# Kernel optimization log

Measured on AMD Instinct MI355X. Metric: run time of the kernel, lower is better.

Reference implementation:

```python
import jax, jax.numpy as jnp
import numpy as np


def get_rel_pos(q_size, k_size, rel_pos):
    # sizes are static python ints; rel_pos has length 2*max(q_size,k_size)-1
    q_ratio = max(k_size / q_size, 1.0)
    k_ratio = max(q_size / k_size, 1.0)
    dist = (np.arange(q_size)[:, None] * q_ratio
            - (np.arange(k_size)[None, :] + (1.0 - k_size)) * k_ratio).astype(np.int64)
    return rel_pos[dist]  # [q_size, k_size, head_dim]


def decomposed_rel_pos_3d(qh, q_thw, k_thw, rel_pos_t, rel_pos_h, rel_pos_w):
    # qh: [B, Q, n_heads, head_dim]
    q_t, q_h, q_w = q_thw
    k_t, k_h, k_w = k_thw
    Rt = get_rel_pos(q_t, k_t, rel_pos_t)
    Rh = get_rel_pos(q_h, k_h, rel_pos_h)
    Rw = get_rel_pos(q_w, k_w, rel_pos_w)
    B = qh.shape[0]
    n, c = qh.shape[2], qh.shape[3]
    q6 = qh.reshape(B, q_t, q_h, q_w, n, c)
    rel_t = jnp.einsum('bthwnc,tkc->bnthwk', q6, Rt)
    rel_h = jnp.einsum('bthwnc,hkc->bnthwk', q6, Rh)
    rel_w = jnp.einsum('bthwnc,wkc->bnthwk', q6, Rw)
    bias = (rel_t[:, :, :, :, :, :, None, None]
            + rel_h[:, :, :, :, :, None, :, None]
            + rel_w[:, :, :, :, :, None, None, :])
    return bias.reshape(B, n, q_t * q_h * q_w, k_t * k_h * k_w)


def setup_inputs() -> dict:
    key = jax.random.key(0)
    ks = jax.random.split(key, 16)
    B, dim, num_heads = 2, 768, 12
    head_dim = dim // num_heads
    q_thw = (8, 14, 14)
    k_thw = (8, 14, 14)
    Q = q_thw[0] * q_thw[1] * q_thw[2]
    K = k_thw[0] * k_thw[1] * k_thw[2]
    s = 0.02
    inp = {
        'q': jax.random.normal(ks[0], (B, Q, dim), jnp.float32),
        'k': jax.random.normal(ks[1], (B, K, dim), jnp.float32),
        'Wq': jax.random.normal(ks[2], (dim, dim), jnp.float32) * s,
        'bq': jnp.zeros((dim,), jnp.float32),
        'Wk': jax.random.normal(ks[3], (dim, dim), jnp.float32) * s,
        'bk': jnp.zeros((dim,), jnp.float32),
        'Wv': jax.random.normal(ks[4], (dim, dim), jnp.float32) * s,
        'bv': jnp.zeros((dim,), jnp.float32),
        'Wo': jax.random.normal(ks[5], (dim, dim), jnp.float32) * s,
        'bo': jnp.zeros((dim,), jnp.float32),
        'rel_pos_t': jax.random.normal(ks[6], (2 * max(q_thw[0], k_thw[0]) - 1, head_dim), jnp.float32) * s,
        'rel_pos_h': jax.random.normal(ks[7], (2 * max(q_thw[1], k_thw[1]) - 1, head_dim), jnp.float32) * s,
        'rel_pos_w': jax.random.normal(ks[8], (2 * max(q_thw[2], k_thw[2]) - 1, head_dim), jnp.float32) * s,
        'q_t': q_thw[0], 'q_h': q_thw[1], 'q_w': q_thw[2],
        'k_t': k_thw[0], 'k_h': k_thw[1], 'k_w': k_thw[2],
    }
    return inp


def reference(q, k, Wq, bq, Wk, bk, Wv, bv, Wo, bo,
              rel_pos_t, rel_pos_h, rel_pos_w,
              q_t, q_h, q_w, k_t, k_h, k_w):
    B, Q, dim = q.shape
    num_heads = 12
    c = dim // num_heads
    scale = 1.0 / np.sqrt(c).astype(np.float32)
    qh = (q @ Wq.T + bq).reshape(B, -1, num_heads, c)   # [B,Q,n,c]
    vh = (k @ Wv.T + bv).reshape(B, -1, num_heads, c)   # [B,K,n,c]
    kh = (k @ Wk.T + bk).reshape(B, -1, num_heads, c)   # [B,K,n,c]
    bias = decomposed_rel_pos_3d(qh, (q_t, q_h, q_w), (k_t, k_h, k_w),
                                 rel_pos_t, rel_pos_h, rel_pos_w)  # [B,n,Q,K]
    scores = jnp.einsum('bqnc,bknc->bnqk', qh, kh) * scale + bias
    attn = jax.nn.softmax(scores, axis=-1)
    out = jnp.einsum('bnqk,bknc->bqnc', attn, vh).reshape(B, Q, dim)
    return out @ Wo.T + bo
```

## Files before the change

### kernel.cpp

```cpp
#include <hip/hip_runtime.h>
#include <math.h>

typedef __bf16 bf16_t;
typedef __bf16 bf16x4 __attribute__((ext_vector_type(4)));
typedef __bf16 bf16x8 __attribute__((ext_vector_type(8)));
typedef float floatx4 __attribute__((ext_vector_type(4)));

#define MFMA16(A, B, C) __builtin_amdgcn_mfma_f32_16x16x32_bf16((A), (B), (C), 0, 0, 0)

static constexpr int BB  = 2;
static constexpr int NH  = 12;
static constexpr int HD  = 64;
static constexpr int DIM = 768;
static constexpr int QS  = 1568;
static constexpr int KS  = 1568;
static constexpr int KSP = 1664;
static constexpr int MROWS = BB * QS;
static constexpr int KT  = 32;
static constexpr int TD  = 80;

static constexpr float LOG2E = 1.4426950408889634f;
static constexpr float SCALE_L2E = 0.125f * LOG2E;

__device__ __forceinline__ void async16(const void* g, void* l) {
    __builtin_amdgcn_global_load_lds(
        (const __attribute__((address_space(1))) unsigned int*)g,
        (__attribute__((address_space(3))) unsigned int*)l, 16, 0, 0);
}

__global__ __launch_bounds__(256) void cvt_w(
    const float* __restrict__ q, const float* __restrict__ k,
    const float* __restrict__ wq, const float* __restrict__ wk,
    const float* __restrict__ wv, const float* __restrict__ wo,
    const float* __restrict__ rpt, const float* __restrict__ rph,
    const float* __restrict__ rpw,
    bf16_t* __restrict__ Wb, bf16_t* __restrict__ qb, bf16_t* __restrict__ kb,
    bf16_t* __restrict__ koh, bf16_t* __restrict__ Tt)
{
    const int NW4 = DIM * DIM / 4;
    const int NX4 = MROWS * DIM / 4;
    int i = blockIdx.x * 256 + threadIdx.x;
    if (i < 4 * NW4) {
        const int w = i / NW4;
        const int off = i - w * NW4;
        const float* src = (w == 0) ? wq : (w == 1) ? wk : (w == 2) ? wv : wo;
        floatx4 v = ((const floatx4*)src)[off];
        bf16x4 o;
#pragma unroll
        for (int r = 0; r < 4; ++r) o[r] = (bf16_t)v[r];
        ((bf16x4*)(Wb + (size_t)w * DIM * DIM))[off] = o;
        return;
    }
    i -= 4 * NW4;
    if (i < 2 * NX4) {
        const float* src = (i < NX4) ? q : k;
        bf16_t* dst = (i < NX4) ? qb : kb;
        const int off = (i < NX4) ? i : i - NX4;
        floatx4 v = ((const floatx4*)src)[off];
        bf16x4 o;
#pragma unroll
        for (int r = 0; r < 4; ++r) o[r] = (bf16_t)v[r];
        ((bf16x4*)dst)[off] = o;
        return;
    }
    i -= 2 * NX4;
    if (i < KS) {
        const int key = i;
        const int tk = key / 196;
        const int rem = key - tk * 196;
        const int hk = rem / 14;
        const int wk_ = rem - hk * 14;
#pragma unroll
        for (int c8 = 0; c8 < 8; ++c8) {
            bf16x8 v;
#pragma unroll
            for (int j = 0; j < 8; ++j) {
                const int e = c8 * 8 + j;
                const float f = (e == tk || e == 8 + hk || e == 22 + wk_) ? 1.f : 0.f;
                v[j] = (bf16_t)f;
            }
            *(bf16x8*)(koh + (size_t)key * 64 + c8 * 8) = v;
        }
        return;
    }
    i -= KS;
    if (i < TD * 8) {
        const int d = i >> 3;
        const int c8 = (i & 7) * 8;
        bf16x8 v;
#pragma unroll
        for (int j = 0; j < 8; ++j) {
            const int c = c8 + j;
            float f = 0.f;
            if (d < 15)      f = LOG2E * rpt[(size_t)d * 64 + c];
            else if (d < 42) f = LOG2E * rph[(size_t)(d - 15) * 64 + c];
            else if (d < 69) f = LOG2E * rpw[(size_t)(d - 42) * 64 + c];
            v[j] = (bf16_t)f;
        }
        *(bf16x8*)(Tt + (size_t)d * 64 + c8) = v;
    }
}

__global__ __launch_bounds__(256) void gemm_qkv(
    const bf16_t* __restrict__ qb, const bf16_t* __restrict__ kb,
    const bf16_t* __restrict__ Wb,
    const float* __restrict__ bq, const float* __restrict__ bk,
    const float* __restrict__ bv,
    bf16_t* __restrict__ qhP, bf16_t* __restrict__ khP, bf16_t* __restrict__ vT)
{
    __shared__ __align__(16) bf16_t Asa[128 * 64];
    __shared__ __align__(16) bf16_t Asb[128 * 64];
    __shared__ __align__(16) bf16_t Bsa[64 * 64];
    __shared__ __align__(16) bf16_t Bsb[64 * 64];

    const int tid   = threadIdx.x;
    const int lane  = tid & 63;
    const int wave  = tid >> 6;
    const int row16 = lane & 15;
    const int quad  = lane >> 4;
    const int wm    = wave & 1;
    const int wn    = wave >> 1;
    const int m0 = blockIdx.x * 128;
    const int yb = blockIdx.y;
    const int proj = yb / 12;
    const int n0 = (yb - proj * 12) * 64;

    const bf16_t* X = (proj == 0) ? qb : kb;
    const bf16_t* W = Wb + (size_t)proj * DIM * DIM;
    const float* bias = (proj == 0) ? bq : (proj == 1) ? bk : bv;
    const float osc = (proj == 1) ? SCALE_L2E : 1.0f;

    floatx4 acc[4][2];
#pragma unroll
    for (int mt = 0; mt < 4; ++mt)
#pragma unroll
        for (int nt = 0; nt < 2; ++nt) acc[mt][nt] = (floatx4){0.f, 0.f, 0.f, 0.f};

    auto stage = [&](int k0, bf16_t* An, bf16_t* Bn) {
#pragma unroll
        for (int p = 0; p < 4; ++p) {
            const int s = p * 256 + tid;
            const int row = s >> 3, c = s & 7;
            const int g = c ^ (row & 7);
            const int rowc = min(m0 + row, MROWS - 1);
            async16(X + (size_t)rowc * DIM + k0 + g * 8, An + s * 8);
        }
#pragma unroll
        for (int p = 0; p < 2; ++p) {
            const int s = p * 256 + tid;
            const int row = s >> 3, c = s & 7;
            const int g = c ^ (row & 7);
            async16(W + (size_t)(n0 + row) * DIM + k0 + g * 8, Bn + s * 8);
        }
    };

    auto body = [&](int k0, const bf16_t* Ac, const bf16_t* Bc,
                    bf16_t* An, bf16_t* Bn, bool pf) {
        __syncthreads();
        if (pf) stage(k0 + 64, An, Bn);
#pragma unroll
        for (int h = 0; h < 2; ++h) {
            const int pa = (h * 4 + quad) ^ (row16 & 7);
            bf16x8 aF[4], bF[2];
#pragma unroll
            for (int mt = 0; mt < 4; ++mt) {
                const int rowA = wm * 64 + mt * 16 + row16;
                aF[mt] = *(const bf16x8*)&Ac[rowA * 64 + pa * 8];
            }
#pragma unroll
            for (int nt = 0; nt < 2; ++nt) {
                const int rowB = wn * 32 + nt * 16 + row16;
                bF[nt] = *(const bf16x8*)&Bc[rowB * 64 + pa * 8];
            }
#pragma unroll
            for (int mt = 0; mt < 4; ++mt)
#pragma unroll
                for (int nt = 0; nt < 2; ++nt)
                    acc[mt][nt] = MFMA16(aF[mt], bF[nt], acc[mt][nt]);
        }
    };

    stage(0, Asa, Bsa);
    for (int ii = 0; ii < 6; ++ii) {
        const int k0 = ii * 128;
        body(k0,      Asa, Bsa, Asb, Bsb, true);
        body(k0 + 64, Asb, Bsb, Asa, Bsa, k0 + 128 < DIM);
    }

#pragma unroll
    for (int nt = 0; nt < 2; ++nt) {
        const int col = n0 + wn * 32 + nt * 16 + row16;
        const int head = col >> 6, cl = col & 63;
        const float bv_ = bias[col];
#pragma unroll
        for (int mt = 0; mt < 4; ++mt) {
            const int row0 = m0 + wm * 64 + mt * 16 + quad * 4;
            if (row0 < MROWS) {
                const int bb = (row0 >= KS) ? 1 : 0;
                const int key0 = row0 - bb * KS;
                if (proj == 2) {
                    bf16x4 pv;
#pragma unroll
                    for (int r = 0; r < 4; ++r) pv[r] = (bf16_t)(acc[mt][nt][r] + bv_);
                    *(bf16x4*)&vT[((size_t)(bb * NH + head) * 64 + cl) * KSP + key0] = pv;
                } else {
                    bf16_t* dst = (proj == 0) ? qhP : khP;
#pragma unroll
                    for (int r = 0; r < 4; ++r)
                        dst[((size_t)(bb * NH + head) * KS + key0 + r) * 64 + cl] =
                            (bf16_t)((acc[mt][nt][r] + bv_) * osc);
                }
            }
        }
    }
}

__global__ __launch_bounds__(256) void qext(
    const bf16_t* __restrict__ qhP, const bf16_t* __restrict__ Tt,
    bf16_t* __restrict__ Qe)
{
    __shared__ float Gs[64][81];

    const int tid   = threadIdx.x;
    const int lane  = tid & 63;
    const int wave  = tid >> 6;
    const int row16 = lane & 15;
    const int quad  = lane >> 4;
    const int m0 = blockIdx.x * 64;

    const bf16_t* ap = qhP + (size_t)(m0 + wave * 16 + row16) * 64 + quad * 8;
    bf16x8 a0 = *(const bf16x8*)(ap);
    bf16x8 a1 = *(const bf16x8*)(ap + 32);

    floatx4 acc[5];
#pragma unroll
    for (int t = 0; t < 5; ++t) {
        const bf16_t* tp = Tt + (size_t)(t * 16 + row16) * 64 + quad * 8;
        floatx4 s = (floatx4){0.f, 0.f, 0.f, 0.f};
        s = MFMA16(a0, *(const bf16x8*)(tp), s);
        s = MFMA16(a1, *(const bf16x8*)(tp + 32), s);
        acc[t] = s;
    }
#pragma unroll
    for (int t = 0; t < 5; ++t)
#pragma unroll
        for (int r = 0; r < 4; ++r)
            Gs[wave * 16 + quad * 4 + r][t * 16 + row16] = acc[t][r];
    __syncthreads();

#pragma unroll
    for (int ii = 0; ii < 16; ++ii) {
        const int i = ii * 256 + tid;
        const int row = i >> 6, e = i & 63;
        const int grow = m0 + row;
        const int qg = grow % QS;
        const int tq = qg / 196;
        const int rem = qg - tq * 196;
        const int hq = rem / 14;
        const int wq = rem - hq * 14;
        int d;
        if (e < 8)       d = tq - e + 7;
        else if (e < 22) d = 15 + hq - (e - 8) + 13;
        else             d = 42 + wq - (e - 22) + 13;
        const float val = (e < 36) ? Gs[row][d] : 0.f;
        Qe[(size_t)grow * 64 + e] = (bf16_t)val;
    }
}

__global__ __launch_bounds__(256, 2) void attn_fused(
    const bf16_t* __restrict__ qhP, const bf16_t* __restrict__ Qe,
    const bf16_t* __restrict__ khP, const bf16_t* __restrict__ koh,
    const bf16_t* __restrict__ vT, bf16_t* __restrict__ ao)
{
    __shared__ __align__(16) bf16_t KsA[32 * 128];
    __shared__ __align__(16) bf16_t KsB[32 * 128];
    __shared__ __align__(16) bf16_t VsA[64 * 32];
    __shared__ __align__(16) bf16_t VsB[64 * 32];
    __shared__ __align__(16) bf16_t Pl[4 * 16 * 40];

    const int tid   = threadIdx.x;
    const int lane  = tid & 63;
    const int wave  = tid >> 6;
    const int row16 = lane & 15;
    const int quad  = lane >> 4;

    const int L = blockIdx.x;
    const int xcd = L & 7;
    const int j = L >> 3;
    const int bn = xcd * 3 + (j % 3);
    const int q0 = (j / 3) * 64;
    const int b = bn / NH;
    const int n = bn - b * NH;

    const int qrow = min(q0 + wave * 16 + row16, QS - 1);
    const bf16_t* qp = qhP + ((size_t)bn * QS + qrow) * 64 + quad * 8;
    const bf16_t* qe = Qe  + ((size_t)bn * QS + qrow) * 64 + quad * 8;
    bf16x8 aQ0 = *(const bf16x8*)(qp);
    bf16x8 aQ1 = *(const bf16x8*)(qp + 32);
    bf16x8 aQ2 = *(const bf16x8*)(qe);
    bf16x8 aQ3 = *(const bf16x8*)(qe + 32);

    floatx4 O[4];
#pragma unroll
    for (int ct = 0; ct < 4; ++ct) O[ct] = (floatx4){0.f, 0.f, 0.f, 0.f};
    float lsum[4] = {0.f, 0.f, 0.f, 0.f};

    const bf16_t* khb = khP + (size_t)bn * KS * 64;
    const bf16_t* vTb = vT + (size_t)bn * 64 * KSP;
    const int pbase = wave * 16 * 40;
    const int sw3 = row16 & 7;
    const int sw2 = (row16 >> 1) & 3;

    auto stageKV = [&](int k0, bf16_t* Kn, bf16_t* Vn) {
#pragma unroll
        for (int p = 0; p < 2; ++p) {
            const int s = p * 256 + tid;
            const int row = s >> 4, c = s & 15;
            const int l = c ^ (row & 7);
            const bf16_t* src = (l < 8)
                ? khb + (size_t)(k0 + row) * 64 + l * 8
                : koh + (size_t)(k0 + row) * 64 + (l - 8) * 8;
            async16(src, Kn + s * 8);
        }
        {
            const int row = tid >> 2, c = tid & 3;
            const int l = c ^ ((row >> 1) & 3);
            async16(vTb + (size_t)row * KSP + k0 + l * 8, Vn + tid * 8);
        }
    };

    auto iter = [&](int ki, const bf16_t* Kc, const bf16_t* Vc,
                    bf16_t* Kn, bf16_t* Vn, bool pf) {
        const int k0 = ki * KT;
        __syncthreads();
        if (pf) stageKV(k0 + KT, Kn, Vn);

        floatx4 S[2];
#pragma unroll
        for (int t = 0; t < 2; ++t) {
            const bf16_t* kp_ = &Kc[(t * 16 + row16) * 128];
            floatx4 s = (floatx4){0.f, 0.f, 0.f, 0.f};
            s = MFMA16(aQ0, *(const bf16x8*)&kp_[((0 + quad) ^ sw3) * 8], s);
            s = MFMA16(aQ1, *(const bf16x8*)&kp_[((4 + quad) ^ sw3) * 8], s);
            s = MFMA16(aQ2, *(const bf16x8*)&kp_[((8 + quad) ^ sw3) * 8], s);
            s = MFMA16(aQ3, *(const bf16x8*)&kp_[((12 + quad) ^ sw3) * 8], s);
            S[t] = s;
        }

#pragma unroll
        for (int t = 0; t < 2; ++t) {
#pragma unroll
            for (int r = 0; r < 4; ++r) {
                float p = __builtin_amdgcn_exp2f(S[t][r]);
                lsum[r] += p;
                Pl[pbase + (quad * 4 + r) * 40 + t * 16 + row16] = (bf16_t)p;
            }
        }

        bf16x8 aP = *(const bf16x8*)&Pl[pbase + row16 * 40 + quad * 8];
#pragma unroll
        for (int ct = 0; ct < 4; ++ct) {
            bf16x8 bV = *(const bf16x8*)&Vc[(ct * 16 + row16) * 32 + (quad ^ sw2) * 8];
            O[ct] = MFMA16(aP, bV, O[ct]);
        }
    };

    stageKV(0, KsA, VsA);
#pragma unroll 1
    for (int kp2 = 0; kp2 < 24; ++kp2) {
        iter(2 * kp2,     KsA, VsA, KsB, VsB, true);
        iter(2 * kp2 + 1, KsB, VsB, KsA, VsA, true);
    }
    iter(48, KsA, VsA, KsB, VsB, false);

    float inv[4];
#pragma unroll
    for (int r = 0; r < 4; ++r) {
        float l = lsum[r];
        l += __shfl_xor(l, 1);
        l += __shfl_xor(l, 2);
        l += __shfl_xor(l, 4);
        l += __shfl_xor(l, 8);
        inv[r] = 1.f / l;
    }
#pragma unroll
    for (int ct = 0; ct < 4; ++ct) {
        const int c = n * HD + ct * 16 + row16;
#pragma unroll
        for (int r = 0; r < 4; ++r) {
            const int qr = q0 + wave * 16 + quad * 4 + r;
            if (qr < QS)
                ao[(size_t)(b * QS + qr) * DIM + c] = (bf16_t)(O[ct][r] * inv[r]);
        }
    }
}

__global__ __launch_bounds__(256) void gemm_o(
    const bf16_t* __restrict__ X, const bf16_t* __restrict__ W,
    const float* __restrict__ bias, float* __restrict__ Y)
{
    __shared__ __align__(16) bf16_t Asa[64 * 64];
    __shared__ __align__(16) bf16_t Asb[64 * 64];
    __shared__ __align__(16) bf16_t Bsa[64 * 64];
    __shared__ __align__(16) bf16_t Bsb[64 * 64];

    const int tid   = threadIdx.x;
    const int lane  = tid & 63;
    const int wave  = tid >> 6;
    const int row16 = lane & 15;
    const int quad  = lane >> 4;
    const int m0 = blockIdx.x * 64;
    const int n0 = blockIdx.y * 64;

    floatx4 acc[4];
#pragma unroll
    for (int nt = 0; nt < 4; ++nt) acc[nt] = (floatx4){0.f, 0.f, 0.f, 0.f};

    auto stage = [&](int k0, bf16_t* An, bf16_t* Bn) {
#pragma unroll
        for (int p = 0; p < 2; ++p) {
            const int s = p * 256 + tid;
            const int row = s >> 3, pc = s & 7;
            const int g = pc ^ (row & 7);
            async16(X + (size_t)(m0 + row) * DIM + k0 + g * 8, An + s * 8);
            async16(W + (size_t)(n0 + row) * DIM + k0 + g * 8, Bn + s * 8);
        }
    };

    auto body = [&](int k0, const bf16_t* Ac, const bf16_t* Bc,
                    bf16_t* An, bf16_t* Bn, bool pf) {
        __syncthreads();
        if (pf) stage(k0 + 64, An, Bn);
#pragma unroll
        for (int h = 0; h < 2; ++h) {
            const int lc = h * 4 + quad;
            const int pa = lc ^ (row16 & 7);
            const int rowA = wave * 16 + row16;
            bf16x8 aF = *(const bf16x8*)&Ac[rowA * 64 + pa * 8];
#pragma unroll
            for (int nt = 0; nt < 4; ++nt) {
                bf16x8 bF = *(const bf16x8*)&Bc[(nt * 16 + row16) * 64 + pa * 8];
                acc[nt] = MFMA16(aF, bF, acc[nt]);
            }
        }
    };

    stage(0, Asa, Bsa);
    for (int ii = 0; ii < 6; ++ii) {
        const int k0 = ii * 128;
        body(k0,      Asa, Bsa, Asb, Bsb, true);
        body(k0 + 64, Asb, Bsb, Asa, Bsa, k0 + 128 < DIM);
    }

#pragma unroll
    for (int nt = 0; nt < 4; ++nt) {
        const int col = n0 + nt * 16 + row16;
        const float bv = bias[col];
#pragma unroll
        for (int r = 0; r < 4; ++r) {
            const int row = m0 + wave * 16 + quad * 4 + r;
            Y[(size_t)row * DIM + col] = acc[nt][r] + bv;
        }
    }
}

extern "C" void kernel_launch(void* const* d_in, const int* in_sizes, int n_in,
                              void* d_out, int out_size, void* d_ws, size_t ws_size,
                              hipStream_t stream) {
    const float* q   = (const float*)d_in[0];
    const float* k   = (const float*)d_in[1];
    const float* Wq  = (const float*)d_in[2];
    const float* bq  = (const float*)d_in[3];
    const float* Wk  = (const float*)d_in[4];
    const float* bk  = (const float*)d_in[5];
    const float* Wv  = (const float*)d_in[6];
    const float* bv  = (const float*)d_in[7];
    const float* Wo  = (const float*)d_in[8];
    const float* bo  = (const float*)d_in[9];
    const float* rpt = (const float*)d_in[10];
    const float* rph = (const float*)d_in[11];
    const float* rpw = (const float*)d_in[12];

    bf16_t* qhP  = (bf16_t*)d_ws;
    bf16_t* khP  = qhP  + (size_t)MROWS * DIM;
    bf16_t* vT   = khP  + (size_t)MROWS * DIM;
    bf16_t* QeKb = vT   + (size_t)BB * NH * HD * KSP;
    bf16_t* aoQb = QeKb + (size_t)MROWS * DIM;
    bf16_t* koh  = aoQb + (size_t)MROWS * DIM;
    bf16_t* Tt   = koh  + (size_t)KS * 64;
    bf16_t* Wb   = Tt   + (size_t)TD * 64;

    const int NW4 = DIM * DIM / 4;
    const int NX4 = MROWS * DIM / 4;
    const int NCVT = 4 * NW4 + 2 * NX4 + KS + TD * 8;
    cvt_w<<<(NCVT + 255) / 256, 256, 0, stream>>>(
        q, k, Wq, Wk, Wv, Wo, rpt, rph, rpw, Wb, aoQb, QeKb, koh, Tt);

    gemm_qkv<<<dim3(25, 36), 256, 0, stream>>>(
        aoQb, QeKb, Wb, bq, bk, bv, qhP, khP, vT);

    qext<<<(BB * NH * QS) / 64, 256, 0, stream>>>(qhP, Tt, QeKb);

    attn_fused<<<dim3(8 * 3 * 25), 256, 0, stream>>>(
        qhP, QeKb, khP, koh, vT, aoQb);

    gemm_o<<<dim3(MROWS / 64, DIM / 64), 256, 0, stream>>>(
        aoQb, Wb + (size_t)3 * DIM * DIM, bo, (float*)d_out);
}
```

Baseline: 206.3 us.

## Widen attention key tile to 64 with 2x2 wave split and LDS reduction

The fused attention kernel now processes 64 keys per step instead of 32. Each wave handles 32 query rows by 32 keys, so every K fragment loaded from LDS feeds two query row groups and every V fragment feeds two MFMAs. Partial O and row sums from the two key-group waves are merged through LDS at the end. Keys past the sequence end are clamped on load and masked to zero probability, and the padded tail of V^T is zeroed in the conversion kernel. The aim is fewer barriers and more operand reuse, at the cost of more LDS per block, higher register pressure, and an extra reduction step.

```diff
diff --git a/kernel.cpp b/kernel.cpp
--- a/kernel.cpp
+++ b/kernel.cpp
@@ -16,7 +16,7 @@
 static constexpr int KS  = 1568;
 static constexpr int KSP = 1664;
 static constexpr int MROWS = BB * QS;
-static constexpr int KT  = 32;
+static constexpr int KT  = 64;
 static constexpr int TD  = 80;
 
 static constexpr float LOG2E = 1.4426950408889634f;
@@ -35,10 +35,11 @@
     const float* __restrict__ rpt, const float* __restrict__ rph,
     const float* __restrict__ rpw,
     bf16_t* __restrict__ Wb, bf16_t* __restrict__ qb, bf16_t* __restrict__ kb,
-    bf16_t* __restrict__ koh, bf16_t* __restrict__ Tt)
+    bf16_t* __restrict__ koh, bf16_t* __restrict__ Tt, bf16_t* __restrict__ vT)
 {
     const int NW4 = DIM * DIM / 4;
     const int NX4 = MROWS * DIM / 4;
+    const int PADC = (KSP - KS) / 8;
     int i = blockIdx.x * 256 + threadIdx.x;
     if (i < 4 * NW4) {
         const int w = i / NW4;
@@ -98,6 +99,16 @@
             v[j] = (bf16_t)f;
         }
         *(bf16x8*)(Tt + (size_t)d * 64 + c8) = v;
+        return;
+    }
+    i -= TD * 8;
+    if (i < BB * NH * HD * PADC) {
+        const int row = i / PADC;
+        const int ch  = i - row * PADC;
+        bf16x8 z;
+#pragma unroll
+        for (int r = 0; r < 8; ++r) z[r] = (bf16_t)0.f;
+        *(bf16x8*)(vT + (size_t)row * KSP + KS + ch * 8) = z;
     }
 }
 
@@ -272,17 +283,19 @@
     const bf16_t* __restrict__ khP, const bf16_t* __restrict__ koh,
     const bf16_t* __restrict__ vT, bf16_t* __restrict__ ao)
 {
-    __shared__ __align__(16) bf16_t KsA[32 * 128];
-    __shared__ __align__(16) bf16_t KsB[32 * 128];
-    __shared__ __align__(16) bf16_t VsA[64 * 32];
-    __shared__ __align__(16) bf16_t VsB[64 * 32];
-    __shared__ __align__(16) bf16_t Pl[4 * 16 * 40];
+    __shared__ __align__(16) bf16_t KsA[64 * 128];
+    __shared__ __align__(16) bf16_t KsB[64 * 128];
+    __shared__ __align__(16) bf16_t VsA[64 * 64];
+    __shared__ __align__(16) bf16_t VsB[64 * 64];
+    __shared__ __align__(16) bf16_t Pl[4 * 16 * 72];
 
     const int tid   = threadIdx.x;
     const int lane  = tid & 63;
     const int wave  = tid >> 6;
     const int row16 = lane & 15;
     const int quad  = lane >> 4;
+    const int qg    = wave & 1;
+    const int kg    = wave >> 1;
 
     const int L = blockIdx.x;
     const int xcd = L & 7;
@@ -292,40 +305,48 @@
     const int b = bn / NH;
     const int n = bn - b * NH;
 
-    const int qrow = min(q0 + wave * 16 + row16, QS - 1);
-    const bf16_t* qp = qhP + ((size_t)bn * QS + qrow) * 64 + quad * 8;
-    const bf16_t* qe = Qe  + ((size_t)bn * QS + qrow) * 64 + quad * 8;
-    bf16x8 aQ0 = *(const bf16x8*)(qp);
-    bf16x8 aQ1 = *(const bf16x8*)(qp + 32);
-    bf16x8 aQ2 = *(const bf16x8*)(qe);
-    bf16x8 aQ3 = *(const bf16x8*)(qe + 32);
-
-    floatx4 O[4];
-#pragma unroll
-    for (int ct = 0; ct < 4; ++ct) O[ct] = (floatx4){0.f, 0.f, 0.f, 0.f};
-    float lsum[4] = {0.f, 0.f, 0.f, 0.f};
+    bf16x8 aQ[2][4];
+#pragma unroll
+    for (int rg = 0; rg < 2; ++rg) {
+        const int qrow = min(q0 + qg * 32 + rg * 16 + row16, QS - 1);
+        const bf16_t* qp = qhP + ((size_t)bn * QS + qrow) * 64 + quad * 8;
+        const bf16_t* qe = Qe  + ((size_t)bn * QS + qrow) * 64 + quad * 8;
+        aQ[rg][0] = *(const bf16x8*)(qp);
+        aQ[rg][1] = *(const bf16x8*)(qp + 32);
+        aQ[rg][2] = *(const bf16x8*)(qe);
+        aQ[rg][3] = *(const bf16x8*)(qe + 32);
+    }
+
+    floatx4 O[2][4];
+#pragma unroll
+    for (int rg = 0; rg < 2; ++rg)
+#pragma unroll
+        for (int ct = 0; ct < 4; ++ct) O[rg][ct] = (floatx4){0.f, 0.f, 0.f, 0.f};
+    float lsum[2][4] = {{0.f, 0.f, 0.f, 0.f}, {0.f, 0.f, 0.f, 0.f}};
 
     const bf16_t* khb = khP + (size_t)bn * KS * 64;
     const bf16_t* vTb = vT + (size_t)bn * 64 * KSP;
-    const int pbase = wave * 16 * 40;
-    const int sw3 = row16 & 7;
-    const int sw2 = (row16 >> 1) & 3;
+    const int rsw = row16 & 7;
+    const int pbase = qg * 2 * 16 * 72;
 
     auto stageKV = [&](int k0, bf16_t* Kn, bf16_t* Vn) {
 #pragma unroll
-        for (int p = 0; p < 2; ++p) {
+        for (int p = 0; p < 4; ++p) {
             const int s = p * 256 + tid;
             const int row = s >> 4, c = s & 15;
             const int l = c ^ (row & 7);
+            const int rowc = min(k0 + row, KS - 1);
             const bf16_t* src = (l < 8)
-                ? khb + (size_t)(k0 + row) * 64 + l * 8
-                : koh + (size_t)(k0 + row) * 64 + (l - 8) * 8;
+                ? khb + (size_t)rowc * 64 + l * 8
+                : koh + (size_t)rowc * 64 + (l - 8) * 8;
             async16(src, Kn + s * 8);
         }
-        {
-            const int row = tid >> 2, c = tid & 3;
-            const int l = c ^ ((row >> 1) & 3);
-            async16(vTb + (size_t)row * KSP + k0 + l * 8, Vn + tid * 8);
+#pragma unroll
+        for (int p = 0; p < 2; ++p) {
+            const int s = p * 256 + tid;
+            const int row = s >> 3, c = s & 7;
+            const int l = c ^ (row & 7);
+            async16(vTb + (size_t)row * KSP + k0 + l * 8, Vn + s * 8);
         }
     };
 
@@ -335,63 +356,109 @@
         __syncthreads();
         if (pf) stageKV(k0 + KT, Kn, Vn);
 
-        floatx4 S[2];
+        floatx4 S[2][2];
 #pragma unroll
         for (int t = 0; t < 2; ++t) {
-            const bf16_t* kp_ = &Kc[(t * 16 + row16) * 128];
-            floatx4 s = (floatx4){0.f, 0.f, 0.f, 0.f};
-            s = MFMA16(aQ0, *(const bf16x8*)&kp_[((0 + quad) ^ sw3) * 8], s);
-            s = MFMA16(aQ1, *(const bf16x8*)&kp_[((4 + quad) ^ sw3) * 8], s);
-            s = MFMA16(aQ2, *(const bf16x8*)&kp_[((8 + quad) ^ sw3) * 8], s);
-            s = MFMA16(aQ3, *(const bf16x8*)&kp_[((12 + quad) ^ sw3) * 8], s);
-            S[t] = s;
+            const int krow = kg * 32 + t * 16 + row16;
+            const bf16_t* kp_ = &Kc[krow * 128];
+            bf16x8 kf[4];
+#pragma unroll
+            for (int c = 0; c < 4; ++c)
+                kf[c] = *(const bf16x8*)&kp_[((c * 4 + quad) ^ rsw) * 8];
+#pragma unroll
+            for (int rg = 0; rg < 2; ++rg) {
+                floatx4 s = (floatx4){0.f, 0.f, 0.f, 0.f};
+                s = MFMA16(aQ[rg][0], kf[0], s);
+                s = MFMA16(aQ[rg][1], kf[1], s);
+                s = MFMA16(aQ[rg][2], kf[2], s);
+                s = MFMA16(aQ[rg][3], kf[3], s);
+                S[rg][t] = s;
+            }
         }
 
 #pragma unroll
         for (int t = 0; t < 2; ++t) {
-#pragma unroll
-            for (int r = 0; r < 4; ++r) {
-                float p = __builtin_amdgcn_exp2f(S[t][r]);
-                lsum[r] += p;
-                Pl[pbase + (quad * 4 + r) * 40 + t * 16 + row16] = (bf16_t)p;
-            }
-        }
-
-        bf16x8 aP = *(const bf16x8*)&Pl[pbase + row16 * 40 + quad * 8];
+            const int key = k0 + kg * 32 + t * 16 + row16;
+            const bool ok = (key < KS);
+#pragma unroll
+            for (int rg = 0; rg < 2; ++rg) {
+#pragma unroll
+                for (int r = 0; r < 4; ++r) {
+                    float p = __builtin_amdgcn_exp2f(S[rg][t][r]);
+                    p = ok ? p : 0.f;
+                    lsum[rg][r] += p;
+                    Pl[pbase + rg * 1152 + (quad * 4 + r) * 72 + kg * 32 + t * 16 + row16]
+                        = (bf16_t)p;
+                }
+            }
+        }
+
+        bf16x8 aP[2];
+#pragma unroll
+        for (int rg = 0; rg < 2; ++rg)
+            aP[rg] = *(const bf16x8*)&Pl[pbase + rg * 1152 + row16 * 72 + kg * 32 + quad * 8];
 #pragma unroll
         for (int ct = 0; ct < 4; ++ct) {
-            bf16x8 bV = *(const bf16x8*)&Vc[(ct * 16 + row16) * 32 + (quad ^ sw2) * 8];
-            O[ct] = MFMA16(aP, bV, O[ct]);
+            const bf16x8 bV =
+                *(const bf16x8*)&Vc[(ct * 16 + row16) * 64 + ((kg * 4 + quad) ^ rsw) * 8];
+            O[0][ct] = MFMA16(aP[0], bV, O[0][ct]);
+            O[1][ct] = MFMA16(aP[1], bV, O[1][ct]);
         }
     };
 
     stageKV(0, KsA, VsA);
 #pragma unroll 1
-    for (int kp2 = 0; kp2 < 24; ++kp2) {
+    for (int kp2 = 0; kp2 < 12; ++kp2) {
         iter(2 * kp2,     KsA, VsA, KsB, VsB, true);
         iter(2 * kp2 + 1, KsB, VsB, KsA, VsA, true);
     }
-    iter(48, KsA, VsA, KsB, VsB, false);
-
-    float inv[4];
-#pragma unroll
-    for (int r = 0; r < 4; ++r) {
-        float l = lsum[r];
-        l += __shfl_xor(l, 1);
-        l += __shfl_xor(l, 2);
-        l += __shfl_xor(l, 4);
-        l += __shfl_xor(l, 8);
-        inv[r] = 1.f / l;
-    }
-#pragma unroll
-    for (int ct = 0; ct < 4; ++ct) {
-        const int c = n * HD + ct * 16 + row16;
-#pragma unroll
-        for (int r = 0; r < 4; ++r) {
-            const int qr = q0 + wave * 16 + quad * 4 + r;
-            if (qr < QS)
-                ao[(size_t)(b * QS + qr) * DIM + c] = (bf16_t)(O[ct][r] * inv[r]);
-        }
+    iter(24, KsA, VsA, KsB, VsB, false);
+
+    __syncthreads();
+    float* Oex = (float*)KsA;
+    float* Lex = (float*)VsA;
+    if (kg == 1) {
+#pragma unroll
+        for (int rg = 0; rg < 2; ++rg) {
+#pragma unroll
+            for (int ct = 0; ct < 4; ++ct)
+                *(floatx4*)&Oex[((qg * 64 + lane) * 8 + rg * 4 + ct) * 4] = O[rg][ct];
+#pragma unroll
+            for (int r = 0; r < 4; ++r)
+                Lex[(qg * 64 + lane) * 8 + rg * 4 + r] = lsum[rg][r];
+        }
+    }
+    __syncthreads();
+    if (kg == 0) {
+        float inv[2][4];
+#pragma unroll
+        for (int rg = 0; rg < 2; ++rg) {
+#pragma unroll
+            for (int ct = 0; ct < 4; ++ct)
+                O[rg][ct] += *(const floatx4*)&Oex[((qg * 64 + lane) * 8 + rg * 4 + ct) * 4];
+#pragma unroll
+            for (int r = 0; r < 4; ++r) {
+                float l = lsum[rg][r] + Lex[(qg * 64 + lane) * 8 + rg * 4 + r];
+                l += __shfl_xor(l, 1);
+                l += __shfl_xor(l, 2);
+                l += __shfl_xor(l, 4);
+                l += __shfl_xor(l, 8);
+                inv[rg][r] = 1.f / l;
+            }
+        }
+#pragma unroll
+        for (int rg = 0; rg < 2; ++rg)
+#pragma unroll
+            for (int ct = 0; ct < 4; ++ct) {
+                const int c = n * HD + ct * 16 + row16;
+#pragma unroll
+                for (int r = 0; r < 4; ++r) {
+                    const int qr = q0 + qg * 32 + rg * 16 + quad * 4 + r;
+                    if (qr < QS)
+                        ao[(size_t)(b * QS + qr) * DIM + c] =
+                            (bf16_t)(O[rg][ct][r] * inv[rg][r]);
+                }
+            }
     }
 }
 
@@ -492,9 +559,10 @@
 
     const int NW4 = DIM * DIM / 4;
     const int NX4 = MROWS * DIM / 4;
-    const int NCVT = 4 * NW4 + 2 * NX4 + KS + TD * 8;
+    const int PADC = (KSP - KS) / 8;
+    const int NCVT = 4 * NW4 + 2 * NX4 + KS + TD * 8 + BB * NH * HD * PADC;
     cvt_w<<<(NCVT + 255) / 256, 256, 0, stream>>>(
-        q, k, Wq, Wk, Wv, Wo, rpt, rph, rpw, Wb, aoQb, QeKb, koh, Tt);
+        q, k, Wq, Wk, Wv, Wo, rpt, rph, rpw, Wb, aoQb, QeKb, koh, Tt, vT);
 
     gemm_qkv<<<dim3(25, 36), 256, 0, stream>>>(
         aoQb, QeKb, Wb, bq, bk, bv, qhP, khP, vT);
```

Result: slower. 211.5 us (+2.5%).

## Halve attention block to 32 query rows with 128 threads and split MFMA chains

Applied to the files above, without the earlier changes.

The attention kernel now uses 2 waves covering 32 query rows per block instead of 4 waves covering 64, so it launches 49 row tiles per head instead of 25 and drops the partial last tile and its bounds checks, since 1568 divides evenly by 32. The QK^T accumulation is split into two independent MFMA chains to shorten the dependency latency. The V padding columns are now zeroed explicitly in the conversion kernel. The smaller blocks are meant to improve occupancy and load balance across CUs, at the cost of reloading each K/V tile from memory twice as often.

```diff
diff --git a/kernel.cpp b/kernel.cpp
--- a/kernel.cpp
+++ b/kernel.cpp
@@ -35,10 +35,11 @@
     const float* __restrict__ rpt, const float* __restrict__ rph,
     const float* __restrict__ rpw,
     bf16_t* __restrict__ Wb, bf16_t* __restrict__ qb, bf16_t* __restrict__ kb,
-    bf16_t* __restrict__ koh, bf16_t* __restrict__ Tt)
+    bf16_t* __restrict__ koh, bf16_t* __restrict__ Tt, bf16_t* __restrict__ vT)
 {
     const int NW4 = DIM * DIM / 4;
     const int NX4 = MROWS * DIM / 4;
+    const int PADC = (KSP - KS) / 8;
     int i = blockIdx.x * 256 + threadIdx.x;
     if (i < 4 * NW4) {
         const int w = i / NW4;
@@ -98,6 +99,16 @@
             v[j] = (bf16_t)f;
         }
         *(bf16x8*)(Tt + (size_t)d * 64 + c8) = v;
+        return;
+    }
+    i -= TD * 8;
+    if (i < BB * NH * HD * PADC) {
+        const int row = i / PADC;
+        const int ch  = i - row * PADC;
+        bf16x8 z;
+#pragma unroll
+        for (int r = 0; r < 8; ++r) z[r] = (bf16_t)0.f;
+        *(bf16x8*)(vT + (size_t)row * KSP + KS + ch * 8) = z;
     }
 }
 
@@ -267,7 +278,7 @@
     }
 }
 
-__global__ __launch_bounds__(256, 2) void attn_fused(
+__global__ __launch_bounds__(128, 3) void attn_fused(
     const bf16_t* __restrict__ qhP, const bf16_t* __restrict__ Qe,
     const bf16_t* __restrict__ khP, const bf16_t* __restrict__ koh,
     const bf16_t* __restrict__ vT, bf16_t* __restrict__ ao)
@@ -276,7 +287,7 @@
     __shared__ __align__(16) bf16_t KsB[32 * 128];
     __shared__ __align__(16) bf16_t VsA[64 * 32];
     __shared__ __align__(16) bf16_t VsB[64 * 32];
-    __shared__ __align__(16) bf16_t Pl[4 * 16 * 40];
+    __shared__ __align__(16) bf16_t Pl[2 * 16 * 40];
 
     const int tid   = threadIdx.x;
     const int lane  = tid & 63;
@@ -288,11 +299,11 @@
     const int xcd = L & 7;
     const int j = L >> 3;
     const int bn = xcd * 3 + (j % 3);
-    const int q0 = (j / 3) * 64;
+    const int q0 = (j / 3) * 32;
     const int b = bn / NH;
     const int n = bn - b * NH;
 
-    const int qrow = min(q0 + wave * 16 + row16, QS - 1);
+    const int qrow = q0 + wave * 16 + row16;
     const bf16_t* qp = qhP + ((size_t)bn * QS + qrow) * 64 + quad * 8;
     const bf16_t* qe = Qe  + ((size_t)bn * QS + qrow) * 64 + quad * 8;
     bf16x8 aQ0 = *(const bf16x8*)(qp);
@@ -313,8 +324,8 @@
 
     auto stageKV = [&](int k0, bf16_t* Kn, bf16_t* Vn) {
 #pragma unroll
-        for (int p = 0; p < 2; ++p) {
-            const int s = p * 256 + tid;
+        for (int p = 0; p < 4; ++p) {
+            const int s = p * 128 + tid;
             const int row = s >> 4, c = s & 15;
             const int l = c ^ (row & 7);
             const bf16_t* src = (l < 8)
@@ -322,10 +333,12 @@
                 : koh + (size_t)(k0 + row) * 64 + (l - 8) * 8;
             async16(src, Kn + s * 8);
         }
-        {
-            const int row = tid >> 2, c = tid & 3;
+#pragma unroll
+        for (int p = 0; p < 2; ++p) {
+            const int s = p * 128 + tid;
+            const int row = s >> 2, c = s & 3;
             const int l = c ^ ((row >> 1) & 3);
-            async16(vTb + (size_t)row * KSP + k0 + l * 8, Vn + tid * 8);
+            async16(vTb + (size_t)row * KSP + k0 + l * 8, Vn + s * 8);
         }
     };
 
@@ -339,12 +352,13 @@
 #pragma unroll
         for (int t = 0; t < 2; ++t) {
             const bf16_t* kp_ = &Kc[(t * 16 + row16) * 128];
-            floatx4 s = (floatx4){0.f, 0.f, 0.f, 0.f};
-            s = MFMA16(aQ0, *(const bf16x8*)&kp_[((0 + quad) ^ sw3) * 8], s);
-            s = MFMA16(aQ1, *(const bf16x8*)&kp_[((4 + quad) ^ sw3) * 8], s);
-            s = MFMA16(aQ2, *(const bf16x8*)&kp_[((8 + quad) ^ sw3) * 8], s);
-            s = MFMA16(aQ3, *(const bf16x8*)&kp_[((12 + quad) ^ sw3) * 8], s);
-            S[t] = s;
+            floatx4 sA = (floatx4){0.f, 0.f, 0.f, 0.f};
+            floatx4 sB = (floatx4){0.f, 0.f, 0.f, 0.f};
+            sA = MFMA16(aQ0, *(const bf16x8*)&kp_[((0 + quad) ^ sw3) * 8], sA);
+            sB = MFMA16(aQ2, *(const bf16x8*)&kp_[((8 + quad) ^ sw3) * 8], sB);
+            sA = MFMA16(aQ1, *(const bf16x8*)&kp_[((4 + quad) ^ sw3) * 8], sA);
+            sB = MFMA16(aQ3, *(const bf16x8*)&kp_[((12 + quad) ^ sw3) * 8], sB);
+            S[t] = sA + sB;
         }
 
 #pragma unroll
@@ -389,8 +403,7 @@
 #pragma unroll
         for (int r = 0; r < 4; ++r) {
             const int qr = q0 + wave * 16 + quad * 4 + r;
-            if (qr < QS)
-                ao[(size_t)(b * QS + qr) * DIM + c] = (bf16_t)(O[ct][r] * inv[r]);
+            ao[(size_t)(b * QS + qr) * DIM + c] = (bf16_t)(O[ct][r] * inv[r]);
         }
     }
 }
@@ -492,16 +505,17 @@
 
     const int NW4 = DIM * DIM / 4;
     const int NX4 = MROWS * DIM / 4;
-    const int NCVT = 4 * NW4 + 2 * NX4 + KS + TD * 8;
+    const int PADC = (KSP - KS) / 8;
+    const int NCVT = 4 * NW4 + 2 * NX4 + KS + TD * 8 + BB * NH * HD * PADC;
     cvt_w<<<(NCVT + 255) / 256, 256, 0, stream>>>(
-        q, k, Wq, Wk, Wv, Wo, rpt, rph, rpw, Wb, aoQb, QeKb, koh, Tt);
+        q, k, Wq, Wk, Wv, Wo, rpt, rph, rpw, Wb, aoQb, QeKb, koh, Tt, vT);
 
     gemm_qkv<<<dim3(25, 36), 256, 0, stream>>>(
         aoQb, QeKb, Wb, bq, bk, bv, qhP, khP, vT);
 
     qext<<<(BB * NH * QS) / 64, 256, 0, stream>>>(qhP, Tt, QeKb);
 
-    attn_fused<<<dim3(8 * 3 * 25), 256, 0, stream>>>(
+    attn_fused<<<dim3(8 * 3 * 49), 128, 0, stream>>>(
         qhP, QeKb, khP, koh, vT, aoQb);
 
     gemm_o<<<dim3(MROWS / 64, DIM / 64), 256, 0, stream>>>(
```

After: 213.9 us. 1.04x slower.

## Make attention kernel persistent with atomic work queue and MFMA priority hints

Applied to the files above, without the earlier changes.

The attention kernel becomes persistent: 512 blocks pull (head, query-tile) units from a global atomic counter instead of launching 600 blocks statically mapped to XCDs. The counter is reset in the conversion kernel, which now also zeroes the padded tail of the transposed V buffer. s_setprio raises wave priority around the MFMA sections. The aim is to smooth the tail wave and load imbalance, at the cost of losing the XCD-aware L2 locality mapping and adding an atomic plus a barrier per unit.

```diff
diff --git a/kernel.cpp b/kernel.cpp
--- a/kernel.cpp
+++ b/kernel.cpp
@@ -18,6 +18,7 @@
 static constexpr int MROWS = BB * QS;
 static constexpr int KT  = 32;
 static constexpr int TD  = 80;
+static constexpr int NUNITS = 24 * 25;
 
 static constexpr float LOG2E = 1.4426950408889634f;
 static constexpr float SCALE_L2E = 0.125f * LOG2E;
@@ -35,11 +36,14 @@
     const float* __restrict__ rpt, const float* __restrict__ rph,
     const float* __restrict__ rpw,
     bf16_t* __restrict__ Wb, bf16_t* __restrict__ qb, bf16_t* __restrict__ kb,
-    bf16_t* __restrict__ koh, bf16_t* __restrict__ Tt)
+    bf16_t* __restrict__ koh, bf16_t* __restrict__ Tt, bf16_t* __restrict__ vT,
+    int* __restrict__ ctr)
 {
     const int NW4 = DIM * DIM / 4;
     const int NX4 = MROWS * DIM / 4;
+    const int PADC = (KSP - KS) / 8;
     int i = blockIdx.x * 256 + threadIdx.x;
+    if (i == 0) *ctr = 0;
     if (i < 4 * NW4) {
         const int w = i / NW4;
         const int off = i - w * NW4;
@@ -98,6 +102,16 @@
             v[j] = (bf16_t)f;
         }
         *(bf16x8*)(Tt + (size_t)d * 64 + c8) = v;
+        return;
+    }
+    i -= TD * 8;
+    if (i < BB * NH * HD * PADC) {
+        const int row = i / PADC;
+        const int ch  = i - row * PADC;
+        bf16x8 z;
+#pragma unroll
+        for (int r = 0; r < 8; ++r) z[r] = (bf16_t)0.f;
+        *(bf16x8*)(vT + (size_t)row * KSP + KS + ch * 8) = z;
     }
 }
 
@@ -270,127 +284,136 @@
 __global__ __launch_bounds__(256, 2) void attn_fused(
     const bf16_t* __restrict__ qhP, const bf16_t* __restrict__ Qe,
     const bf16_t* __restrict__ khP, const bf16_t* __restrict__ koh,
-    const bf16_t* __restrict__ vT, bf16_t* __restrict__ ao)
+    const bf16_t* __restrict__ vT, bf16_t* __restrict__ ao,
+    int* __restrict__ ctr)
 {
     __shared__ __align__(16) bf16_t KsA[32 * 128];
     __shared__ __align__(16) bf16_t KsB[32 * 128];
     __shared__ __align__(16) bf16_t VsA[64 * 32];
     __shared__ __align__(16) bf16_t VsB[64 * 32];
     __shared__ __align__(16) bf16_t Pl[4 * 16 * 40];
+    __shared__ int s_unit;
 
     const int tid   = threadIdx.x;
     const int lane  = tid & 63;
     const int wave  = tid >> 6;
     const int row16 = lane & 15;
     const int quad  = lane >> 4;
-
-    const int L = blockIdx.x;
-    const int xcd = L & 7;
-    const int j = L >> 3;
-    const int bn = xcd * 3 + (j % 3);
-    const int q0 = (j / 3) * 64;
-    const int b = bn / NH;
-    const int n = bn - b * NH;
-
-    const int qrow = min(q0 + wave * 16 + row16, QS - 1);
-    const bf16_t* qp = qhP + ((size_t)bn * QS + qrow) * 64 + quad * 8;
-    const bf16_t* qe = Qe  + ((size_t)bn * QS + qrow) * 64 + quad * 8;
-    bf16x8 aQ0 = *(const bf16x8*)(qp);
-    bf16x8 aQ1 = *(const bf16x8*)(qp + 32);
-    bf16x8 aQ2 = *(const bf16x8*)(qe);
-    bf16x8 aQ3 = *(const bf16x8*)(qe + 32);
-
-    floatx4 O[4];
-#pragma unroll
-    for (int ct = 0; ct < 4; ++ct) O[ct] = (floatx4){0.f, 0.f, 0.f, 0.f};
-    float lsum[4] = {0.f, 0.f, 0.f, 0.f};
-
-    const bf16_t* khb = khP + (size_t)bn * KS * 64;
-    const bf16_t* vTb = vT + (size_t)bn * 64 * KSP;
     const int pbase = wave * 16 * 40;
     const int sw3 = row16 & 7;
     const int sw2 = (row16 >> 1) & 3;
 
-    auto stageKV = [&](int k0, bf16_t* Kn, bf16_t* Vn) {
-#pragma unroll
-        for (int p = 0; p < 2; ++p) {
-            const int s = p * 256 + tid;
-            const int row = s >> 4, c = s & 15;
-            const int l = c ^ (row & 7);
-            const bf16_t* src = (l < 8)
-                ? khb + (size_t)(k0 + row) * 64 + l * 8
-                : koh + (size_t)(k0 + row) * 64 + (l - 8) * 8;
-            async16(src, Kn + s * 8);
-        }
-        {
-            const int row = tid >> 2, c = tid & 3;
-            const int l = c ^ ((row >> 1) & 3);
-            async16(vTb + (size_t)row * KSP + k0 + l * 8, Vn + tid * 8);
-        }
-    };
-
-    auto iter = [&](int ki, const bf16_t* Kc, const bf16_t* Vc,
-                    bf16_t* Kn, bf16_t* Vn, bool pf) {
-        const int k0 = ki * KT;
+    for (;;) {
+        if (tid == 0) s_unit = atomicAdd(ctr, 1);
         __syncthreads();
-        if (pf) stageKV(k0 + KT, Kn, Vn);
-
-        floatx4 S[2];
-#pragma unroll
-        for (int t = 0; t < 2; ++t) {
-            const bf16_t* kp_ = &Kc[(t * 16 + row16) * 128];
-            floatx4 s = (floatx4){0.f, 0.f, 0.f, 0.f};
-            s = MFMA16(aQ0, *(const bf16x8*)&kp_[((0 + quad) ^ sw3) * 8], s);
-            s = MFMA16(aQ1, *(const bf16x8*)&kp_[((4 + quad) ^ sw3) * 8], s);
-            s = MFMA16(aQ2, *(const bf16x8*)&kp_[((8 + quad) ^ sw3) * 8], s);
-            s = MFMA16(aQ3, *(const bf16x8*)&kp_[((12 + quad) ^ sw3) * 8], s);
-            S[t] = s;
-        }
-
-#pragma unroll
-        for (int t = 0; t < 2; ++t) {
+        const int u = s_unit;
+        if (u >= NUNITS) return;
+        const int bn = u / 25;
+        const int q0 = (u - bn * 25) * 64;
+        const int b = bn / NH;
+        const int n = bn - b * NH;
+
+        const int qrow = min(q0 + wave * 16 + row16, QS - 1);
+        const bf16_t* qp = qhP + ((size_t)bn * QS + qrow) * 64 + quad * 8;
+        const bf16_t* qe = Qe  + ((size_t)bn * QS + qrow) * 64 + quad * 8;
+        bf16x8 aQ0 = *(const bf16x8*)(qp);
+        bf16x8 aQ1 = *(const bf16x8*)(qp + 32);
+        bf16x8 aQ2 = *(const bf16x8*)(qe);
+        bf16x8 aQ3 = *(const bf16x8*)(qe + 32);
+
+        floatx4 O[4];
+#pragma unroll
+        for (int ct = 0; ct < 4; ++ct) O[ct] = (floatx4){0.f, 0.f, 0.f, 0.f};
+        float lsum[4] = {0.f, 0.f, 0.f, 0.f};
+
+        const bf16_t* khb = khP + (size_t)bn * KS * 64;
+        const bf16_t* vTb = vT + (size_t)bn * 64 * KSP;
+
+        auto stageKV = [&](int k0, bf16_t* Kn, bf16_t* Vn) {
+#pragma unroll
+            for (int p = 0; p < 2; ++p) {
+                const int s = p * 256 + tid;
+                const int row = s >> 4, c = s & 15;
+                const int l = c ^ (row & 7);
+                const bf16_t* src = (l < 8)
+                    ? khb + (size_t)(k0 + row) * 64 + l * 8
+                    : koh + (size_t)(k0 + row) * 64 + (l - 8) * 8;
+                async16(src, Kn + s * 8);
+            }
+            {
+                const int row = tid >> 2, c = tid & 3;
+                const int l = c ^ ((row >> 1) & 3);
+                async16(vTb + (size_t)row * KSP + k0 + l * 8, Vn + tid * 8);
+            }
+        };
+
+        auto iter = [&](int ki, const bf16_t* Kc, const bf16_t* Vc,
+                        bf16_t* Kn, bf16_t* Vn, bool pf) {
+            const int k0 = ki * KT;
+            __syncthreads();
+            if (pf) stageKV(k0 + KT, Kn, Vn);
+
+            floatx4 S[2];
+            __builtin_amdgcn_s_setprio(1);
+#pragma unroll
+            for (int t = 0; t < 2; ++t) {
+                const bf16_t* kp_ = &Kc[(t * 16 + row16) * 128];
+                floatx4 s = (floatx4){0.f, 0.f, 0.f, 0.f};
+                s = MFMA16(aQ0, *(const bf16x8*)&kp_[((0 + quad) ^ sw3) * 8], s);
+                s = MFMA16(aQ1, *(const bf16x8*)&kp_[((4 + quad) ^ sw3) * 8], s);
+                s = MFMA16(aQ2, *(const bf16x8*)&kp_[((8 + quad) ^ sw3) * 8], s);
+                s = MFMA16(aQ3, *(const bf16x8*)&kp_[((12 + quad) ^ sw3) * 8], s);
+                S[t] = s;
+            }
+            __builtin_amdgcn_s_setprio(0);
+
+#pragma unroll
+            for (int t = 0; t < 2; ++t) {
+#pragma unroll
+                for (int r = 0; r < 4; ++r) {
+                    float p = __builtin_amdgcn_exp2f(S[t][r]);
+                    lsum[r] += p;
+                    Pl[pbase + (quad * 4 + r) * 40 + t * 16 + row16] = (bf16_t)p;
+                }
+            }
+
+            bf16x8 aP = *(const bf16x8*)&Pl[pbase + row16 * 40 + quad * 8];
+            __builtin_amdgcn_s_setprio(1);
+#pragma unroll
+            for (int ct = 0; ct < 4; ++ct) {
+                bf16x8 bV = *(const bf16x8*)&Vc[(ct * 16 + row16) * 32 + (quad ^ sw2) * 8];
+                O[ct] = MFMA16(aP, bV, O[ct]);
+            }
+            __builtin_amdgcn_s_setprio(0);
+        };
+
+        stageKV(0, KsA, VsA);
+#pragma unroll 1
+        for (int kp2 = 0; kp2 < 24; ++kp2) {
+            iter(2 * kp2,     KsA, VsA, KsB, VsB, true);
+            iter(2 * kp2 + 1, KsB, VsB, KsA, VsA, true);
+        }
+        iter(48, KsA, VsA, KsB, VsB, false);
+
+        float inv[4];
+#pragma unroll
+        for (int r = 0; r < 4; ++r) {
+            float l = lsum[r];
+            l += __shfl_xor(l, 1);
+            l += __shfl_xor(l, 2);
+            l += __shfl_xor(l, 4);
+            l += __shfl_xor(l, 8);
+            inv[r] = 1.f / l;
+        }
+#pragma unroll
+        for (int ct = 0; ct < 4; ++ct) {
+            const int c = n * HD + ct * 16 + row16;
 #pragma unroll
             for (int r = 0; r < 4; ++r) {
-                float p = __builtin_amdgcn_exp2f(S[t][r]);
-                lsum[r] += p;
-                Pl[pbase + (quad * 4 + r) * 40 + t * 16 + row16] = (bf16_t)p;
-            }
-        }
-
-        bf16x8 aP = *(const bf16x8*)&Pl[pbase + row16 * 40 + quad * 8];
-#pragma unroll
-        for (int ct = 0; ct < 4; ++ct) {
-            bf16x8 bV = *(const bf16x8*)&Vc[(ct * 16 + row16) * 32 + (quad ^ sw2) * 8];
-            O[ct] = MFMA16(aP, bV, O[ct]);
-        }
-    };
-
-    stageKV(0, KsA, VsA);
-#pragma unroll 1
-    for (int kp2 = 0; kp2 < 24; ++kp2) {
-        iter(2 * kp2,     KsA, VsA, KsB, VsB, true);
-        iter(2 * kp2 + 1, KsB, VsB, KsA, VsA, true);
-    }
-    iter(48, KsA, VsA, KsB, VsB, false);
-
-    float inv[4];
-#pragma unroll
-    for (int r = 0; r < 4; ++r) {
-        float l = lsum[r];
-        l += __shfl_xor(l, 1);
-        l += __shfl_xor(l, 2);
-        l += __shfl_xor(l, 4);
-        l += __shfl_xor(l, 8);
-        inv[r] = 1.f / l;
-    }
-#pragma unroll
-    for (int ct = 0; ct < 4; ++ct) {
-        const int c = n * HD + ct * 16 + row16;
-#pragma unroll
-        for (int r = 0; r < 4; ++r) {
-            const int qr = q0 + wave * 16 + quad * 4 + r;
-            if (qr < QS)
-                ao[(size_t)(b * QS + qr) * DIM + c] = (bf16_t)(O[ct][r] * inv[r]);
+                const int qr = q0 + wave * 16 + quad * 4 + r;
+                if (qr < QS)
+                    ao[(size_t)(b * QS + qr) * DIM + c] = (bf16_t)(O[ct][r] * inv[r]);
+            }
         }
     }
 }
@@ -489,20 +512,22 @@
     bf16_t* koh  = aoQb + (size_t)MROWS * DIM;
     bf16_t* Tt   = koh  + (size_t)KS * 64;
     bf16_t* Wb   = Tt   + (size_t)TD * 64;
+    int*    ctr  = (int*)(Wb + (size_t)4 * DIM * DIM);
 
     const int NW4 = DIM * DIM / 4;
     const int NX4 = MROWS * DIM / 4;
-    const int NCVT = 4 * NW4 + 2 * NX4 + KS + TD * 8;
+    const int PADC = (KSP - KS) / 8;
+    const int NCVT = 4 * NW4 + 2 * NX4 + KS + TD * 8 + BB * NH * HD * PADC;
     cvt_w<<<(NCVT + 255) / 256, 256, 0, stream>>>(
-        q, k, Wq, Wk, Wv, Wo, rpt, rph, rpw, Wb, aoQb, QeKb, koh, Tt);
+        q, k, Wq, Wk, Wv, Wo, rpt, rph, rpw, Wb, aoQb, QeKb, koh, Tt, vT, ctr);
 
     gemm_qkv<<<dim3(25, 36), 256, 0, stream>>>(
         aoQb, QeKb, Wb, bq, bk, bv, qhP, khP, vT);
 
     qext<<<(BB * NH * QS) / 64, 256, 0, stream>>>(qhP, Tt, QeKb);
 
-    attn_fused<<<dim3(8 * 3 * 25), 256, 0, stream>>>(
-        qhP, QeKb, khP, koh, vT, aoQb);
+    attn_fused<<<dim3(512), 256, 0, stream>>>(
+        qhP, QeKb, khP, koh, vT, aoQb, ctr);
 
     gemm_o<<<dim3(MROWS / 64, DIM / 64), 256, 0, stream>>>(
         aoQb, Wb + (size_t)3 * DIM * DIM, bo, (float*)d_out);
```

Measured after the change: 236.4 us. 14.6% more time.
